# Optimization experiments

Hardware: AMD Instinct MI355X
Metric: run time of the kernel (lower is better)

The kernel has to match this reference:

```python
import jax, jax.numpy as jnp
import numpy as np

H = 1024
A = H // 2
B = 32
S = 1024
T = 1024


def setup_inputs() -> dict:
    key = jax.random.key(0)
    ks = jax.random.split(key, 16)
    sc = 0.02
    inp = {
        "hidden": jax.random.normal(ks[0], (1, B, H), jnp.float32),
        "encoder_hiddens": jax.random.normal(ks[1], (S, B, H), jnp.float32),
        "h0_s": jax.random.normal(ks[2], (T, B, H), jnp.float32),
        "ax": jax.random.uniform(ks[3], (B, S, 1), jnp.float32),
        # weights: torch Linear(in,out,bias=False) -> W has shape [out,in], y = x @ W.T
        "W1": jax.random.normal(ks[4], (A, H), jnp.float32) * sc,
        "W2": jax.random.normal(ks[5], (A, H), jnp.float32) * sc,
        "W3": jax.random.normal(ks[6], (A, 1), jnp.float32) * sc,
        "W4": jax.random.normal(ks[7], (1, 3 * A), jnp.float32) * sc,
        "W5": jax.random.normal(ks[8], (A, H), jnp.float32) * sc,
        "W6": jax.random.normal(ks[9], (A, H), jnp.float32) * sc,
        "W7": jax.random.normal(ks[10], (A, H), jnp.float32) * sc,
        "W8": jax.random.normal(ks[11], (1, 3 * A), jnp.float32) * sc,
        "W9": jax.random.normal(ks[12], (H, H), jnp.float32) * sc,
        "W10": jax.random.normal(ks[13], (H, H), jnp.float32) * sc,
        "W11": jax.random.normal(ks[14], (1, 2 * H), jnp.float32) * sc,
    }
    return inp


def reference(hidden, encoder_hiddens, h0_s, ax,
              W1, W2, W3, W4, W5, W6, W7, W8, W9, W10, W11):
    h = hidden[0]  # [B,H], hidden.squeeze(0)

    # ---- encoder (x) attention with coverage, vectorized over S ----
    wx = jnp.einsum('sbh,ah->sba', encoder_hiddens, W1)          # [S,B,A]
    wxy = h @ W2.T                                               # [B,A]
    # Linear3 on ax[:, j] ([B,1]): outer product with W3 column
    wxr = ax[:, :, 0][:, :, None] * W3[:, 0][None, None, :]       # [B,S,A]
    wxr = jnp.transpose(wxr, (1, 0, 2))                           # [S,B,A]
    cat_x = jnp.tanh(jnp.concatenate(
        [wx, jnp.broadcast_to(wxy, (S,) + wxy.shape), wxr], axis=-1))  # [S,B,3A]
    exi = jnp.einsum('sbc,oc->bso', cat_x, W4)                    # [B,S,1]
    axi = jax.nn.softmax(exi, axis=1)                             # [B,S,1]
    cxi = jnp.einsum('bs,sbh->bh', axi[:, :, 0], encoder_hiddens)  # [B,H]
    ax_new = ax + axi

    # ---- decoder-history (t) attention, vectorized over T ----
    wt = jnp.einsum('tbh,ah->tba', h0_s, W5)                      # [T,B,A]
    wtx = cxi @ W6.T                                              # [B,A]
    wty = h @ W7.T                                                # [B,A]
    Tn = h0_s.shape[0]
    cat_t = jnp.tanh(jnp.concatenate(
        [wt,
         jnp.broadcast_to(wtx, (Tn,) + wtx.shape),
         jnp.broadcast_to(wty, (Tn,) + wty.shape)], axis=-1))     # [T,B,3A]
    eti = jnp.einsum('tbc,oc->bto', cat_t, W8)                    # [B,T,1]
    ati = jax.nn.softmax(eti, axis=1)
    cti = jnp.einsum('bt,tbh->bh', ati[:, :, 0], h0_s)            # [B,H]

    # ---- gated fusion ----
    gxi = jnp.tanh(cxi @ W9.T)
    gti = jnp.tanh(cti @ W10.T)
    zi = jax.nn.sigmoid(jnp.concatenate([cxi, cti], axis=1) @ W11.T)  # [B,1]
    ci = zi * gxi + (1.0 - zi) * gti                              # [B,H]
    return ci, ax_new
```

## Files before the change

### kernel.cpp

```cpp
#include <hip/hip_runtime.h>
#include <hip/hip_bf16.h>

#define HH 1024
#define AA 512
#define BB 32
#define SS 1024
#define TN 1024
#define M_ENC (SS*BB)
#define M_TOT ((SS+TN)*BB)
#define NCH 8

typedef __attribute__((ext_vector_type(8))) short short8;
typedef __attribute__((ext_vector_type(4))) float f4;

union bfu { __hip_bfloat16 h; unsigned short u; };
__device__ __forceinline__ unsigned short f2b(float x) {
  bfu t; t.h = __float2bfloat16(x); return t.u;
}
__device__ __forceinline__ float tanh_fast(float x) {
  float e = __expf(2.f * x);
  return 1.f - 2.f / (e + 1.f);
}

__global__ void wprep(const float* __restrict__ W, unsigned short* __restrict__ Wc) {
  const int t = blockIdx.x * 256 + threadIdx.x;
  const int lane = t & 63;
  const int rg = (t >> 6) & 31;
  const int kb = t >> 11;
  const int row = rg * 16 + (lane & 15);
  const int k = kb * 32 + ((lane >> 4) << 3);
  const float* src = W + (size_t)row * HH + k;
  f4 v0 = *(const f4*)(src);
  f4 v1 = *(const f4*)(src + 4);
  short8 o;
  o[0] = f2b(v0[0]); o[1] = f2b(v0[1]); o[2] = f2b(v0[2]); o[3] = f2b(v0[3]);
  o[4] = f2b(v1[0]); o[5] = f2b(v1[1]); o[6] = f2b(v1[2]); o[7] = f2b(v1[3]);
  *(short8*)(Wc + (size_t)t * 8) = o;
}

__global__ __launch_bounds__(1024, 4)
void e1_gemm(const float* __restrict__ enc, const float* __restrict__ h0,
             const unsigned short* __restrict__ W1c, const unsigned short* __restrict__ W5c,
             const float* __restrict__ W4, const float* __restrict__ W8,
             float* __restrict__ e1) {
  const int wg   = blockIdx.x;
  const int tid  = threadIdx.x;
  const int lane = tid & 63;
  const int wave = tid >> 6;
  const int rowg = wave >> 3;
  const int colg = wave & 7;
  const int l15  = lane & 15;
  const int lg   = lane >> 4;

  const bool is_enc = (wg * 128) < M_ENC;
  const float* __restrict__ Xg = is_enc ? enc : h0;
  const unsigned short* __restrict__ Wc = is_enc ? W1c : W5c;
  const float* __restrict__ Vg = is_enc ? W4 : W8;
  const int row0 = is_enc ? wg * 128 : wg * 128 - M_ENC;

  __shared__ char lds_raw[2 * 40960];
  float* lred = (float*)lds_raw;

  float vvv[4];
#pragma unroll
  for (int cf = 0; cf < 4; ++cf) vvv[cf] = Vg[colg * 64 + cf * 16 + l15];

  f4 acc[4][4];
#pragma unroll
  for (int i = 0; i < 4; ++i)
#pragma unroll
    for (int j = 0; j < 4; ++j) acc[i][j] = (f4){0.f, 0.f, 0.f, 0.f};

  const int arow  = tid >> 2;
  const int kslot = tid & 3;
  const int acol  = kslot ^ ((arow >> 1) & 3);
  const float* aSrc = Xg + (size_t)(row0 + arow) * HH + kslot * 8;
  const int aDst = arow * 64 + acol * 16;

  const int aRd = (rowg * 64 + l15) * 64 + ((lg ^ ((l15 >> 1) & 3)) << 4);
  const int bRd = colg * 4096 + lane * 16;

#define BGLL(buf, kb_) do {                                                   \
    _Pragma("unroll")                                                         \
    for (int p_ = 0; p_ < 2; ++p_) {                                          \
      const int idx_ = p_ * 1024 + tid;                                       \
      const char* gB_ = (const char*)Wc + (size_t)(kb_) * 32768 + idx_ * 16;  \
      char* lB_ = lds_raw + (buf) * 40960 + 8192 + idx_ * 16;                 \
      __builtin_amdgcn_global_load_lds(                                       \
          (const __attribute__((address_space(1))) void*)gB_,                 \
          (__attribute__((address_space(3))) void*)lB_, 16, 0, 0);            \
    }                                                                         \
  } while (0)

#define AWRITE(buf, v0_, v1_) do {                                            \
    short8 o_;                                                                \
    o_[0] = f2b(v0_[0]); o_[1] = f2b(v0_[1]);                                 \
    o_[2] = f2b(v0_[2]); o_[3] = f2b(v0_[3]);                                 \
    o_[4] = f2b(v1_[0]); o_[5] = f2b(v1_[1]);                                 \
    o_[6] = f2b(v1_[2]); o_[7] = f2b(v1_[3]);                                 \
    *(short8*)(lds_raw + (buf) * 40960 + aDst) = o_;                          \
  } while (0)

  f4 a0n, a1n;
  if (tid < 512) { a0n = *(const f4*)(aSrc); a1n = *(const f4*)(aSrc + 4); }
  BGLL(0, 0);
  if (tid < 512) AWRITE(0, a0n, a1n);
  __syncthreads();

  int cur = 0;
#pragma unroll 1
  for (int kb = 0; kb < 32; ++kb) {
    if (kb < 31) {
      if (tid < 512) {
        a0n = *(const f4*)(aSrc + (kb + 1) * 32);
        a1n = *(const f4*)(aSrc + (kb + 1) * 32 + 4);
      }
      BGLL(cur ^ 1, kb + 1);
    }

    const char* Ab = lds_raw + cur * 40960;
    const char* Bb = Ab + 8192;

    short8 bfr[4];
#pragma unroll
    for (int cf = 0; cf < 4; ++cf)
      bfr[cf] = *(const short8*)(Bb + bRd + cf * 1024);

#pragma unroll
    for (int rt = 0; rt < 4; ++rt) {
      short8 af = *(const short8*)(Ab + aRd + rt * 1024);
#pragma unroll
      for (int cf = 0; cf < 4; ++cf)
        acc[rt][cf] = __builtin_amdgcn_mfma_f32_16x16x32_bf16(af, bfr[cf], acc[rt][cf], 0, 0, 0);
    }

    if (kb < 31 && tid < 512) AWRITE(cur ^ 1, a0n, a1n);
    __syncthreads();
    cur ^= 1;
  }
#undef BGLL
#undef AWRITE

#pragma unroll
  for (int rt = 0; rt < 4; ++rt) {
    float ps[4] = {0.f, 0.f, 0.f, 0.f};
#pragma unroll
    for (int cf = 0; cf < 4; ++cf) {
      const float w = vvv[cf];
#pragma unroll
      for (int r = 0; r < 4; ++r) ps[r] += w * tanh_fast(acc[rt][cf][r]);
    }
#pragma unroll
    for (int r = 0; r < 4; ++r) {
#pragma unroll
      for (int off = 1; off < 16; off <<= 1) ps[r] += __shfl_xor(ps[r], off);
    }
    if (l15 == 0) {
#pragma unroll
      for (int r = 0; r < 4; ++r)
        lred[colg * 128 + rowg * 64 + rt * 16 + lg * 4 + r] = ps[r];
    }
  }
  __syncthreads();
  if (tid < 128) {
    float s = 0.f;
#pragma unroll
    for (int c = 0; c < 8; ++c) s += lred[c * 128 + tid];
    e1[(size_t)wg * 128 + tid] = s;
  }
}

__global__ void exf_kernel(const float* __restrict__ e1, const float* __restrict__ ax,
                           const float* __restrict__ W3, const float* __restrict__ W4,
                           float* __restrict__ exf) {
  __shared__ float w3s[AA], w4r[AA];
  const int tid = threadIdx.x;
  for (int i = tid; i < AA; i += 256) { w3s[i] = W3[i]; w4r[i] = W4[2 * AA + i]; }
  __syncthreads();
  const int b = blockIdx.x >> 2;
  const int s = (blockIdx.x & 3) * 256 + tid;
  const float x = ax[b * SS + s];
  float er = 0.f;
#pragma unroll 8
  for (int a = 0; a < AA; ++a) er += w4r[a] * tanh_fast(x * w3s[a]);
  exf[b * SS + s] = e1[s * BB + b] + er;
}

__global__ void softmax_bs(const float* __restrict__ ein, const float* __restrict__ ax,
                           float* __restrict__ wout, float* __restrict__ axnew) {
  const int b = blockIdx.x, tid = threadIdx.x;
  __shared__ float red[256];
  float loc[4];
  float m = -1e30f;
#pragma unroll
  for (int i = 0; i < 4; ++i) { loc[i] = ein[b * SS + i * 256 + tid]; m = fmaxf(m, loc[i]); }
  red[tid] = m; __syncthreads();
  for (int off = 128; off > 0; off >>= 1) {
    if (tid < off) red[tid] = fmaxf(red[tid], red[tid + off]);
    __syncthreads();
  }
  m = red[0]; __syncthreads();
  float sum = 0.f;
#pragma unroll
  for (int i = 0; i < 4; ++i) { loc[i] = __expf(loc[i] - m); sum += loc[i]; }
  red[tid] = sum; __syncthreads();
  for (int off = 128; off > 0; off >>= 1) {
    if (tid < off) red[tid] += red[tid + off];
    __syncthreads();
  }
  const float inv = 1.f / red[0];
#pragma unroll
  for (int i = 0; i < 4; ++i) {
    const int s = i * 256 + tid;
    const float a_ = loc[i] * inv;
    wout[b * SS + s] = a_;
    axnew[b * SS + s] = ax[b * SS + s] + a_;
  }
}

__global__ void softmax_tb(const float* __restrict__ ein, float* __restrict__ wout) {
  const int b = blockIdx.x, tid = threadIdx.x;
  __shared__ float red[256];
  float loc[4];
  float m = -1e30f;
#pragma unroll
  for (int i = 0; i < 4; ++i) { loc[i] = ein[(i * 256 + tid) * BB + b]; m = fmaxf(m, loc[i]); }
  red[tid] = m; __syncthreads();
  for (int off = 128; off > 0; off >>= 1) {
    if (tid < off) red[tid] = fmaxf(red[tid], red[tid + off]);
    __syncthreads();
  }
  m = red[0]; __syncthreads();
  float sum = 0.f;
#pragma unroll
  for (int i = 0; i < 4; ++i) { loc[i] = __expf(loc[i] - m); sum += loc[i]; }
  red[tid] = sum; __syncthreads();
  for (int off = 128; off > 0; off >>= 1) {
    if (tid < off) red[tid] += red[tid + off];
    __syncthreads();
  }
  const float inv = 1.f / red[0];
#pragma unroll
  for (int i = 0; i < 4; ++i) wout[b * TN + (i * 256 + tid)] = loc[i] * inv;
}

__global__ void wpart(const float* __restrict__ X, const float* __restrict__ w,
                      float* __restrict__ part) {
  const int b = blockIdx.x / NCH, ch = blockIdx.x % NCH;
  const int tid = threadIdx.x;
  __shared__ float ws[SS / NCH];
  if (tid < SS / NCH) ws[tid] = w[b * SS + ch * (SS / NCH) + tid];
  __syncthreads();
  f4 acc = (f4){0.f, 0.f, 0.f, 0.f};
  const float* base = X + ((size_t)(ch * (SS / NCH)) * BB + b) * HH + tid * 4;
#pragma unroll 4
  for (int i = 0; i < SS / NCH; ++i) {
    f4 x = *(const f4*)(base + (size_t)i * BB * HH);
    acc += ws[i] * x;
  }
  *(f4*)&part[((size_t)(b * NCH + ch)) * HH + tid * 4] = acc;
}

__global__ void wreduce(const float* __restrict__ part, float* __restrict__ out) {
  const int idx = blockIdx.x * 256 + threadIdx.x;
  const int b = idx / HH, h = idx % HH;
  float s = 0.f;
#pragma unroll
  for (int ch = 0; ch < NCH; ++ch) s += part[((size_t)(b * NCH + ch)) * HH + h];
  out[idx] = s;
}

__global__ void zi_kernel(const float* __restrict__ cxi, const float* __restrict__ cti,
                          const float* __restrict__ W11, float* __restrict__ zi) {
  const int b = blockIdx.x, tid = threadIdx.x;
  float s = 0.f;
  for (int i = tid; i < HH; i += 256) s += cxi[b * HH + i] * W11[i] + cti[b * HH + i] * W11[HH + i];
  __shared__ float red[4];
  for (int off = 32; off > 0; off >>= 1) s += __shfl_down(s, off);
  if ((tid & 63) == 0) red[tid >> 6] = s;
  __syncthreads();
  if (tid == 0) {
    float t = red[0] + red[1] + red[2] + red[3];
    zi[b] = 1.f / (1.f + __expf(-t));
  }
}

__global__ void ci_kernel(const float* __restrict__ cxi, const float* __restrict__ cti,
                          const float* __restrict__ W9, const float* __restrict__ W10,
                          const float* __restrict__ zi, float* __restrict__ out_ci) {
  const int b = blockIdx.x >> 2, hb = blockIdx.x & 3, tid = threadIdx.x;
  const int h = hb * 256 + tid;
  __shared__ float cx[HH], ct[HH];
  for (int i = tid; i < HH; i += 256) { cx[i] = cxi[b * HH + i]; ct[i] = cti[b * HH + i]; }
  __syncthreads();
  const float* __restrict__ w9r  = W9  + (size_t)h * HH;
  const float* __restrict__ w10r = W10 + (size_t)h * HH;
  float gx = 0.f, gt = 0.f;
  for (int k = 0; k < HH; k += 4) {
    f4 a = *(const f4*)(w9r + k);
    f4 c = *(const f4*)(w10r + k);
    gx += cx[k] * a[0] + cx[k + 1] * a[1] + cx[k + 2] * a[2] + cx[k + 3] * a[3];
    gt += ct[k] * c[0] + ct[k + 1] * c[1] + ct[k + 2] * c[2] + ct[k + 3] * c[3];
  }
  const float z = zi[b];
  out_ci[b * HH + h] = z * tanhf(gx) + (1.f - z) * tanhf(gt);
}

extern "C" void kernel_launch(void* const* d_in, const int* in_sizes, int n_in,
                              void* d_out, int out_size, void* d_ws, size_t ws_size,
                              hipStream_t stream) {
  const float* enc = (const float*)d_in[1];
  const float* h0  = (const float*)d_in[2];
  const float* ax  = (const float*)d_in[3];
  const float* W1  = (const float*)d_in[4];
  const float* W3  = (const float*)d_in[6];
  const float* W4  = (const float*)d_in[7];
  const float* W5  = (const float*)d_in[8];
  const float* W8  = (const float*)d_in[11];
  const float* W9  = (const float*)d_in[12];
  const float* W10 = (const float*)d_in[13];
  const float* W11 = (const float*)d_in[14];
  float* out = (float*)d_out;

  float* w = (float*)d_ws;
  unsigned short* W1c = (unsigned short*)w;
  unsigned short* W5c = (unsigned short*)(w + 262144);
  float* partx = w;
  float* partt = w + 262144;
  float* e1    = w + 524288;
  float* exf   = w + 589824;
  float* axi   = w + 622592;
  float* ati   = w + 655360;
  float* cxi   = w + 688128;
  float* cti   = w + 720896;
  float* zi    = w + 753664;

  wprep<<<256, 256, 0, stream>>>(W1, W1c);
  wprep<<<256, 256, 0, stream>>>(W5, W5c);
  e1_gemm<<<M_TOT / 128, 1024, 0, stream>>>(enc, h0, W1c, W5c, W4, W8, e1);
  exf_kernel<<<BB * 4, 256, 0, stream>>>(e1, ax, W3, W4, exf);
  softmax_bs<<<BB, 256, 0, stream>>>(exf, ax, axi, out + BB * HH);
  softmax_tb<<<BB, 256, 0, stream>>>(e1 + M_ENC, ati);
  wpart<<<BB * NCH, 256, 0, stream>>>(enc, axi, partx);
  wpart<<<BB * NCH, 256, 0, stream>>>(h0, ati, partt);
  wreduce<<<BB * HH / 256, 256, 0, stream>>>(partx, cxi);
  wreduce<<<BB * HH / 256, 256, 0, stream>>>(partt, cti);
  zi_kernel<<<BB, 256, 0, stream>>>(cxi, cti, W11, zi);
  ci_kernel<<<BB * 4, 256, 0, stream>>>(cxi, cti, W9, W10, zi, out);
}
```

Before: 242.3 us.

## Triple-buffer the GEMM K-loop with partial vmcnt waits instead of full syncs

Moves the fused projection-plus-score GEMM from double to triple LDS buffering, prefetching two K-blocks ahead. The per-iteration __syncthreads is replaced by an explicit s_waitcnt vmcnt(2) plus s_barrier, so the newest global_load_lds traffic can stay in flight across the barrier. The V-weight load is deferred until after the loop, which shortens register live ranges. In exchange, LDS use per workgroup grows to about 124 KB, which may limit occupancy, and correctness depends on the hand-set vmcnt count matching the outstanding loads.

```diff
diff --git a/kernel.cpp b/kernel.cpp
--- a/kernel.cpp
+++ b/kernel.cpp
@@ -58,12 +58,8 @@
   const float* __restrict__ Vg = is_enc ? W4 : W8;
   const int row0 = is_enc ? wg * 128 : wg * 128 - M_ENC;
 
-  __shared__ char lds_raw[2 * 40960];
-  float* lred = (float*)lds_raw;
-
-  float vvv[4];
-#pragma unroll
-  for (int cf = 0; cf < 4; ++cf) vvv[cf] = Vg[colg * 64 + cf * 16 + l15];
+  __shared__ char lds_raw[3 * 40960 + 4096];
+  float* lred = (float*)(lds_raw + 3 * 40960);
 
   f4 acc[4][4];
 #pragma unroll
@@ -80,66 +76,84 @@
   const int aRd = (rowg * 64 + l15) * 64 + ((lg ^ ((l15 >> 1) & 3)) << 4);
   const int bRd = colg * 4096 + lane * 16;
 
-#define BGLL(buf, kb_) do {                                                   \
+#define BGLL(bufoff, kb_) do {                                                \
     _Pragma("unroll")                                                         \
     for (int p_ = 0; p_ < 2; ++p_) {                                          \
       const int idx_ = p_ * 1024 + tid;                                       \
       const char* gB_ = (const char*)Wc + (size_t)(kb_) * 32768 + idx_ * 16;  \
-      char* lB_ = lds_raw + (buf) * 40960 + 8192 + idx_ * 16;                 \
+      char* lB_ = lds_raw + (bufoff) + 8192 + idx_ * 16;                      \
       __builtin_amdgcn_global_load_lds(                                       \
           (const __attribute__((address_space(1))) void*)gB_,                 \
           (__attribute__((address_space(3))) void*)lB_, 16, 0, 0);            \
     }                                                                         \
   } while (0)
 
-#define AWRITE(buf, v0_, v1_) do {                                            \
+#define AWRITE(bufoff, v0_, v1_) do {                                         \
     short8 o_;                                                                \
     o_[0] = f2b(v0_[0]); o_[1] = f2b(v0_[1]);                                 \
     o_[2] = f2b(v0_[2]); o_[3] = f2b(v0_[3]);                                 \
     o_[4] = f2b(v1_[0]); o_[5] = f2b(v1_[1]);                                 \
     o_[6] = f2b(v1_[2]); o_[7] = f2b(v1_[3]);                                 \
-    *(short8*)(lds_raw + (buf) * 40960 + aDst) = o_;                          \
+    *(short8*)(lds_raw + (bufoff) + aDst) = o_;                               \
+  } while (0)
+
+#define COMPUTE(bufoff) do {                                                  \
+    const char* Ab_ = lds_raw + (bufoff);                                     \
+    const char* Bb_ = Ab_ + 8192;                                             \
+    short8 bfr_[4];                                                           \
+    _Pragma("unroll")                                                         \
+    for (int cf = 0; cf < 4; ++cf)                                            \
+      bfr_[cf] = *(const short8*)(Bb_ + bRd + cf * 1024);                     \
+    _Pragma("unroll")                                                         \
+    for (int rt = 0; rt < 4; ++rt) {                                          \
+      short8 af_ = *(const short8*)(Ab_ + aRd + rt * 1024);                   \
+      _Pragma("unroll")                                                       \
+      for (int cf = 0; cf < 4; ++cf)                                          \
+        acc[rt][cf] = __builtin_amdgcn_mfma_f32_16x16x32_bf16(af_, bfr_[cf],  \
+                                                     acc[rt][cf], 0, 0, 0);   \
+    }                                                                         \
+  } while (0)
+
+#define STEP_SYNC() do {                                                      \
+    __builtin_amdgcn_sched_barrier(0);                                        \
+    asm volatile("s_waitcnt vmcnt(2) lgkmcnt(0)" ::: "memory");               \
+    __builtin_amdgcn_s_barrier();                                             \
+    __builtin_amdgcn_sched_barrier(0);                                        \
   } while (0)
 
   f4 a0n, a1n;
   if (tid < 512) { a0n = *(const f4*)(aSrc); a1n = *(const f4*)(aSrc + 4); }
   BGLL(0, 0);
   if (tid < 512) AWRITE(0, a0n, a1n);
-  __syncthreads();
-
-  int cur = 0;
+  if (tid < 512) { a0n = *(const f4*)(aSrc + 32); a1n = *(const f4*)(aSrc + 36); }
+  BGLL(40960, 1);
+  if (tid < 512) AWRITE(40960, a0n, a1n);
+  STEP_SYNC();
+
+  int cur = 0, nxt = 40960, nn = 81920;
 #pragma unroll 1
-  for (int kb = 0; kb < 32; ++kb) {
-    if (kb < 31) {
-      if (tid < 512) {
-        a0n = *(const f4*)(aSrc + (kb + 1) * 32);
-        a1n = *(const f4*)(aSrc + (kb + 1) * 32 + 4);
-      }
-      BGLL(cur ^ 1, kb + 1);
+  for (int kb = 0; kb < 30; ++kb) {
+    if (tid < 512) {
+      a0n = *(const f4*)(aSrc + (kb + 2) * 32);
+      a1n = *(const f4*)(aSrc + (kb + 2) * 32 + 4);
     }
-
-    const char* Ab = lds_raw + cur * 40960;
-    const char* Bb = Ab + 8192;
-
-    short8 bfr[4];
-#pragma unroll
-    for (int cf = 0; cf < 4; ++cf)
-      bfr[cf] = *(const short8*)(Bb + bRd + cf * 1024);
-
-#pragma unroll
-    for (int rt = 0; rt < 4; ++rt) {
-      short8 af = *(const short8*)(Ab + aRd + rt * 1024);
-#pragma unroll
-      for (int cf = 0; cf < 4; ++cf)
-        acc[rt][cf] = __builtin_amdgcn_mfma_f32_16x16x32_bf16(af, bfr[cf], acc[rt][cf], 0, 0, 0);
-    }
-
-    if (kb < 31 && tid < 512) AWRITE(cur ^ 1, a0n, a1n);
-    __syncthreads();
-    cur ^= 1;
-  }
+    BGLL(nn, kb + 2);
+    COMPUTE(cur);
+    if (tid < 512) AWRITE(nn, a0n, a1n);
+    STEP_SYNC();
+    int t = cur; cur = nxt; nxt = nn; nn = t;
+  }
+  COMPUTE(cur);
+  __syncthreads();
+  COMPUTE(nxt);
 #undef BGLL
 #undef AWRITE
+#undef COMPUTE
+#undef STEP_SYNC
+
+  float vvv[4];
+#pragma unroll
+  for (int cf = 0; cf < 4; ++cf) vvv[cf] = Vg[colg * 64 + cf * 16 + l15];
 
 #pragma unroll
   for (int rt = 0; rt < 4; ++rt) {
```

Measured after the change: 243.6 us. No clear change (+0.5%).
